# Kernel tuning notes

Hardware: AMD Instinct MI355X
Metric: run time of the kernel (lower is better)

## Reference

```python
import jax, jax.numpy as jnp
import numpy as np
import math

N = 8192  # base points
M = 8192  # target points
FEAT = 5
DESC = 4
HID = 32


def setup_inputs() -> dict:
    key = jax.random.key(0)
    ks = jax.random.split(key, 16)
    s = lambda fan_in: 1.0 / np.sqrt(fan_in)
    return {
        "base_pos": jax.random.normal(ks[0], (N, 2), jnp.float32),
        "base_feat": jax.random.normal(ks[1], (N, FEAT), jnp.float32),
        "base_desc": jax.random.normal(ks[2], (DESC,), jnp.float32),
        "target_pos": jax.random.normal(ks[3], (M, 2), jnp.float32),
        "target_feat": jax.random.normal(ks[4], (M, FEAT), jnp.float32),
        "target_desc": jax.random.normal(ks[5], (DESC,), jnp.float32),
        # NodeWeightNet MLP params (Linear(5,32) -> ReLU -> Linear(32,1))
        "w1": jax.random.uniform(ks[6], (FEAT, HID), jnp.float32, -s(FEAT), s(FEAT)),
        "b1": jax.random.uniform(ks[7], (HID,), jnp.float32, -s(FEAT), s(FEAT)),
        "w2": jax.random.uniform(ks[8], (HID, 1), jnp.float32, -s(HID), s(HID)),
        "b2": jax.random.uniform(ks[9], (1,), jnp.float32, -s(HID), s(HID)),
        # descriptor gate params (Linear(4,32) -> ReLU -> Linear(32,1))
        "g1": jax.random.uniform(ks[10], (DESC, HID), jnp.float32, -s(DESC), s(DESC)),
        "gb1": jax.random.uniform(ks[11], (HID,), jnp.float32, -s(DESC), s(DESC)),
        "g2": jax.random.uniform(ks[12], (HID, 1), jnp.float32, -s(HID), s(HID)),
        "gb2": jax.random.uniform(ks[13], (1,), jnp.float32, -s(HID), s(HID)),
        "log_sigma": jnp.asarray(math.log(0.1), jnp.float32),
        "log_scale": jnp.zeros((2,), jnp.float32),
        "bias": jnp.zeros((1,), jnp.float32),
    }


def _node_weights(feat, w1, b1, w2, b2):
    logits = jax.nn.relu(feat @ w1 + b1) @ w2 + b2  # [N,1]
    w = jax.nn.softplus(logits) + 1e-6
    return (w / w.sum())[:, 0]  # [N], sums to 1


def _mmd_term(x, wx, y, wy, inv_two_sigma2):
    # weighted sum of Gaussian kernel over all pairs, via sq-dist expansion
    d2 = (
        (x * x).sum(-1)[:, None]
        + (y * y).sum(-1)[None, :]
        - 2.0 * (x @ y.T)
    )
    k = jnp.exp(-d2 * inv_two_sigma2)
    return jnp.einsum("i,ij,j->", wx, k, wy)


def reference(base_pos, base_feat, base_desc, target_pos, target_feat, target_desc,
              w1, b1, w2, b2, g1, gb1, g2, gb2, log_sigma, log_scale, bias):
    scale = jnp.exp(log_scale)
    bp = base_pos * scale
    tp = target_pos * scale
    sigma = jnp.exp(log_sigma)
    bw = _node_weights(base_feat, w1, b1, w2, b2)
    tw = _node_weights(target_feat, w1, b1, w2, b2)
    # center=True: subtract each cloud's weighted mean
    bp = bp - (bw[:, None] * bp).sum(0)
    tp = tp - (tw[:, None] * tp).sum(0)
    inv = 1.0 / (2.0 * sigma * sigma)
    loss = (
        _mmd_term(bp, bw, bp, bw, inv)
        - 2.0 * _mmd_term(bp, bw, tp, tw, inv)
        + _mmd_term(tp, tw, tp, tw, inv)
    )
    diff = jnp.abs(base_desc - target_desc)  # [4]
    gate = jax.nn.softplus(jax.nn.relu(diff @ g1 + gb1) @ g2 + gb2) + 1e-6  # [1]
    return loss * gate.squeeze() + bias.squeeze()
```

## Files before the change

kernel.cpp:

```cpp
#include <hip/hip_runtime.h>
#include <math.h>


#define MMD_THREADS 256
#define I_PER_THREAD 4
#define NPTS_PER_BLOCK (MMD_THREADS * I_PER_THREAD)
#define TJ 256

__device__ __forceinline__ float softplusf(float x) {
    return fmaxf(x, 0.0f) + log1pf(expf(-fabsf(x)));
}

__device__ __forceinline__ float fast_exp2(float x) {
#if __has_builtin(__builtin_amdgcn_exp2f)
    return __builtin_amdgcn_exp2f(x);
#else
    return exp2f(x);
#endif
}

__global__ __launch_bounds__(256) void weight_kernel(
    const float* __restrict__ bpos, const float* __restrict__ bfeat,
    const float* __restrict__ tpos, const float* __restrict__ tfeat,
    const float* __restrict__ w1, const float* __restrict__ b1,
    const float* __restrict__ w2, const float* __restrict__ b2,
    const float* __restrict__ log_scale,
    float4* __restrict__ b4, float4* __restrict__ t4,
    float* __restrict__ sums, int n, int m)
{
    int idx = blockIdx.x * 256 + threadIdx.x;
    int total = n + m;
    float w = 0.f, px = 0.f, py = 0.f;
    int cloud = 0;
    if (idx < total) {
        const float* pos; const float* feat; int i;
        if (idx < n) { pos = bpos; feat = bfeat; i = idx; cloud = 0; }
        else         { pos = tpos; feat = tfeat; i = idx - n; cloud = 1; }
        float sx = expf(log_scale[0]);
        float sy = expf(log_scale[1]);
        px = pos[2*i]   * sx;
        py = pos[2*i+1] * sy;
        float f0 = feat[5*i], f1 = feat[5*i+1], f2 = feat[5*i+2],
              f3 = feat[5*i+3], f4 = feat[5*i+4];
        float logit = b2[0];
        #pragma unroll
        for (int h = 0; h < 32; ++h) {
            float a = b1[h];
            a = fmaf(f0, w1[h],      a);
            a = fmaf(f1, w1[32+h],   a);
            a = fmaf(f2, w1[64+h],   a);
            a = fmaf(f3, w1[96+h],   a);
            a = fmaf(f4, w1[128+h],  a);
            a = fmaxf(a, 0.f);
            logit = fmaf(a, w2[h], logit);
        }
        w = softplusf(logit) + 1e-6f;
        float4 v = make_float4(px, py, w, 0.f);
        if (cloud == 0) b4[i] = v; else t4[i] = v;
    }
    float sw = w, swx = w*px, swy = w*py;
    #pragma unroll
    for (int off = 32; off > 0; off >>= 1) {
        sw  += __shfl_down(sw,  off, 64);
        swx += __shfl_down(swx, off, 64);
        swy += __shfl_down(swy, off, 64);
    }
    if ((threadIdx.x & 63) == 0 && idx < total) {
        float* dst = sums + 3 + cloud * 3;
        atomicAdd(dst + 0, sw);
        atomicAdd(dst + 1, swx);
        atomicAdd(dst + 2, swy);
    }
}

__global__ __launch_bounds__(256) void center_kernel(
    float4* __restrict__ b4, float4* __restrict__ t4,
    const float* __restrict__ sums, int n, int m)
{
    int idx = blockIdx.x * 256 + threadIdx.x;
    int total = n + m;
    if (idx >= total) return;
    int cloud = (idx < n) ? 0 : 1;
    float4* arr = cloud ? t4 : b4;
    int i = cloud ? idx - n : idx;
    const float* s = sums + 3 + cloud * 3;
    float sw = s[0];
    float mx = s[1] / sw, my = s[2] / sw;
    float4 v = arr[i];
    arr[i] = make_float4(v.x - mx, v.y - my, v.z / sw, 0.f);
}

__global__ __launch_bounds__(MMD_THREADS) void mmd_kernel(
    const float4* __restrict__ b4, const float4* __restrict__ t4,
    const float* __restrict__ log_sigma,
    float* __restrict__ sums, int n, int m)
{
    int t = blockIdx.z;
    const float4* X; const float4* Y; int nx, ny;
    if (t == 0)      { X = b4; Y = b4; nx = n; ny = n; }
    else if (t == 1) { X = b4; Y = t4; nx = n; ny = m; }
    else             { X = t4; Y = t4; nx = m; ny = m; }
    float sigma = expf(log_sigma[0]);
    float cexp = -1.4426950408889634f / (2.f * sigma * sigma);

    __shared__ float4 ytile[TJ];
    int j0 = blockIdx.y * TJ;
    for (int j = threadIdx.x; j < TJ; j += MMD_THREADS) {
        int jj = j0 + j;
        ytile[j] = (jj < ny) ? Y[jj] : make_float4(0.f, 0.f, 0.f, 0.f);
    }
    __syncthreads();

    float xi[I_PER_THREAD], yi[I_PER_THREAD], wi[I_PER_THREAD], acc[I_PER_THREAD];
    int ibase = blockIdx.x * NPTS_PER_BLOCK + threadIdx.x;
    #pragma unroll
    for (int s = 0; s < I_PER_THREAD; ++s) {
        int ii = ibase + s * MMD_THREADS;
        float4 v = (ii < nx) ? X[ii] : make_float4(0.f, 0.f, 0.f, 0.f);
        xi[s] = v.x; yi[s] = v.y; wi[s] = v.z; acc[s] = 0.f;
    }
    for (int j = 0; j < TJ; ++j) {
        float4 v = ytile[j];
        #pragma unroll
        for (int s = 0; s < I_PER_THREAD; ++s) {
            float dx = xi[s] - v.x;
            float dy = yi[s] - v.y;
            float d2 = fmaf(dy, dy, dx * dx);
            acc[s] = fmaf(v.z, fast_exp2(d2 * cexp), acc[s]);
        }
    }
    float r = 0.f;
    #pragma unroll
    for (int s = 0; s < I_PER_THREAD; ++s) r = fmaf(wi[s], acc[s], r);

    #pragma unroll
    for (int off = 32; off > 0; off >>= 1) r += __shfl_down(r, off, 64);
    __shared__ float wsum[MMD_THREADS / 64];
    int wid = threadIdx.x >> 6;
    if ((threadIdx.x & 63) == 0) wsum[wid] = r;
    __syncthreads();
    if (threadIdx.x == 0) {
        float tot = 0.f;
        #pragma unroll
        for (int k = 0; k < MMD_THREADS / 64; ++k) tot += wsum[k];
        atomicAdd(&sums[t], tot);
    }
}

__global__ void final_kernel(
    const float* __restrict__ bdesc, const float* __restrict__ tdesc,
    const float* __restrict__ g1, const float* __restrict__ gb1,
    const float* __restrict__ g2, const float* __restrict__ gb2,
    const float* __restrict__ bias, const float* __restrict__ sums,
    float* __restrict__ out)
{
    if (threadIdx.x != 0 || blockIdx.x != 0) return;
    float d0 = fabsf(bdesc[0] - tdesc[0]);
    float d1 = fabsf(bdesc[1] - tdesc[1]);
    float d2 = fabsf(bdesc[2] - tdesc[2]);
    float d3 = fabsf(bdesc[3] - tdesc[3]);
    float logit = gb2[0];
    #pragma unroll
    for (int h = 0; h < 32; ++h) {
        float a = gb1[h];
        a = fmaf(d0, g1[h],      a);
        a = fmaf(d1, g1[32+h],   a);
        a = fmaf(d2, g1[64+h],   a);
        a = fmaf(d3, g1[96+h],   a);
        a = fmaxf(a, 0.f);
        logit = fmaf(a, g2[h], logit);
    }
    float gate = softplusf(logit) + 1e-6f;
    float loss = sums[0] - 2.f * sums[1] + sums[2];
    out[0] = loss * gate + bias[0];
}

extern "C" void kernel_launch(void* const* d_in, const int* in_sizes, int n_in,
                              void* d_out, int out_size, void* d_ws, size_t ws_size,
                              hipStream_t stream)
{
    const float* bpos      = (const float*)d_in[0];
    const float* bfeat     = (const float*)d_in[1];
    const float* bdesc     = (const float*)d_in[2];
    const float* tpos      = (const float*)d_in[3];
    const float* tfeat     = (const float*)d_in[4];
    const float* tdesc     = (const float*)d_in[5];
    const float* w1        = (const float*)d_in[6];
    const float* b1        = (const float*)d_in[7];
    const float* w2        = (const float*)d_in[8];
    const float* b2        = (const float*)d_in[9];
    const float* g1        = (const float*)d_in[10];
    const float* gb1       = (const float*)d_in[11];
    const float* g2        = (const float*)d_in[12];
    const float* gb2       = (const float*)d_in[13];
    const float* log_sigma = (const float*)d_in[14];
    const float* log_scale = (const float*)d_in[15];
    const float* bias      = (const float*)d_in[16];
    float* out = (float*)d_out;

    int n = in_sizes[0] / 2;
    int m = in_sizes[3] / 2;

    char* ws = (char*)d_ws;
    float4* b4  = (float4*)ws;
    float4* t4  = (float4*)(ws + (size_t)n * sizeof(float4));
    float* sums = (float*)(ws + (size_t)(n + m) * sizeof(float4));

    hipMemsetAsync(sums, 0, 9 * sizeof(float), stream);

    int total = n + m;
    int wb = (total + 255) / 256;
    weight_kernel<<<wb, 256, 0, stream>>>(bpos, bfeat, tpos, tfeat,
                                          w1, b1, w2, b2, log_scale,
                                          b4, t4, sums, n, m);
    center_kernel<<<wb, 256, 0, stream>>>(b4, t4, sums, n, m);

    int nmax = n > m ? n : m;
    dim3 grid((nmax + NPTS_PER_BLOCK - 1) / NPTS_PER_BLOCK,
              (nmax + TJ - 1) / TJ, 3);
    mmd_kernel<<<grid, MMD_THREADS, 0, stream>>>(b4, t4, log_sigma, sums, n, m);

    final_kernel<<<1, 64, 0, stream>>>(bdesc, tdesc, g1, gb1, g2, gb2,
                                       bias, sums, out);
}
```

Before: 146.6 us.

## Fold sigma into positions, drop center kernel, spread atomics over partial slots

Positions are prescaled by sqrt(log2 e)/sigma so the inner loop computes exp2 of a negated squared distance directly, with no constant multiply. The separate centering pass is removed: the self terms are translation invariant, the cross term applies the difference of the two weighted means, and normalisation by the weight sums moves into the final kernel. The MMD kernel now handles one i-point per thread and reads Y straight from global memory (wave-uniform broadcast) instead of a shared tile, and atomics are spread over 16 partial slots per term. The risk is lower per-thread ILP and fewer points per block, which means more blocks and more reduction overhead.

```diff
diff --git a/kernel.cpp b/kernel.cpp
--- a/kernel.cpp
+++ b/kernel.cpp
@@ -2,10 +2,11 @@
 #include <math.h>
 
 
+#define WK_THREADS 256
 #define MMD_THREADS 256
-#define I_PER_THREAD 4
-#define NPTS_PER_BLOCK (MMD_THREADS * I_PER_THREAD)
-#define TJ 256
+#define IB 256
+#define JB 256
+#define NPART 16
 
 __device__ __forceinline__ float softplusf(float x) {
     return fmaxf(x, 0.0f) + log1pf(expf(-fabsf(x)));
@@ -19,16 +20,16 @@
 #endif
 }
 
-__global__ __launch_bounds__(256) void weight_kernel(
+__global__ __launch_bounds__(WK_THREADS) void weight_kernel(
     const float* __restrict__ bpos, const float* __restrict__ bfeat,
     const float* __restrict__ tpos, const float* __restrict__ tfeat,
     const float* __restrict__ w1, const float* __restrict__ b1,
     const float* __restrict__ w2, const float* __restrict__ b2,
-    const float* __restrict__ log_scale,
+    const float* __restrict__ log_sigma, const float* __restrict__ log_scale,
     float4* __restrict__ b4, float4* __restrict__ t4,
     float* __restrict__ sums, int n, int m)
 {
-    int idx = blockIdx.x * 256 + threadIdx.x;
+    int idx = blockIdx.x * WK_THREADS + threadIdx.x;
     int total = n + m;
     float w = 0.f, px = 0.f, py = 0.f;
     int cloud = 0;
@@ -36,8 +37,10 @@
         const float* pos; const float* feat; int i;
         if (idx < n) { pos = bpos; feat = bfeat; i = idx; cloud = 0; }
         else         { pos = tpos; feat = tfeat; i = idx - n; cloud = 1; }
-        float sx = expf(log_scale[0]);
-        float sy = expf(log_scale[1]);
+        float sigma = expf(log_sigma[0]);
+        float u = 0.8493218003f / sigma;
+        float sx = expf(log_scale[0]) * u;
+        float sy = expf(log_scale[1]) * u;
         px = pos[2*i]   * sx;
         py = pos[2*i+1] * sy;
         float f0 = feat[5*i], f1 = feat[5*i+1], f2 = feat[5*i+2],
@@ -73,65 +76,46 @@
     }
 }
 
-__global__ __launch_bounds__(256) void center_kernel(
-    float4* __restrict__ b4, float4* __restrict__ t4,
-    const float* __restrict__ sums, int n, int m)
-{
-    int idx = blockIdx.x * 256 + threadIdx.x;
-    int total = n + m;
-    if (idx >= total) return;
-    int cloud = (idx < n) ? 0 : 1;
-    float4* arr = cloud ? t4 : b4;
-    int i = cloud ? idx - n : idx;
-    const float* s = sums + 3 + cloud * 3;
-    float sw = s[0];
-    float mx = s[1] / sw, my = s[2] / sw;
-    float4 v = arr[i];
-    arr[i] = make_float4(v.x - mx, v.y - my, v.z / sw, 0.f);
-}
-
 __global__ __launch_bounds__(MMD_THREADS) void mmd_kernel(
     const float4* __restrict__ b4, const float4* __restrict__ t4,
-    const float* __restrict__ log_sigma,
-    float* __restrict__ sums, int n, int m)
+    const float* __restrict__ sums, float* __restrict__ partial,
+    int n, int m)
 {
     int t = blockIdx.z;
     const float4* X; const float4* Y; int nx, ny;
     if (t == 0)      { X = b4; Y = b4; nx = n; ny = n; }
     else if (t == 1) { X = b4; Y = t4; nx = n; ny = m; }
     else             { X = t4; Y = t4; nx = m; ny = m; }
-    float sigma = expf(log_sigma[0]);
-    float cexp = -1.4426950408889634f / (2.f * sigma * sigma);
-
-    __shared__ float4 ytile[TJ];
-    int j0 = blockIdx.y * TJ;
-    for (int j = threadIdx.x; j < TJ; j += MMD_THREADS) {
-        int jj = j0 + j;
-        ytile[j] = (jj < ny) ? Y[jj] : make_float4(0.f, 0.f, 0.f, 0.f);
-    }
-    __syncthreads();
-
-    float xi[I_PER_THREAD], yi[I_PER_THREAD], wi[I_PER_THREAD], acc[I_PER_THREAD];
-    int ibase = blockIdx.x * NPTS_PER_BLOCK + threadIdx.x;
-    #pragma unroll
-    for (int s = 0; s < I_PER_THREAD; ++s) {
-        int ii = ibase + s * MMD_THREADS;
-        float4 v = (ii < nx) ? X[ii] : make_float4(0.f, 0.f, 0.f, 0.f);
-        xi[s] = v.x; yi[s] = v.y; wi[s] = v.z; acc[s] = 0.f;
-    }
-    for (int j = 0; j < TJ; ++j) {
-        float4 v = ytile[j];
-        #pragma unroll
-        for (int s = 0; s < I_PER_THREAD; ++s) {
-            float dx = xi[s] - v.x;
-            float dy = yi[s] - v.y;
-            float d2 = fmaf(dy, dy, dx * dx);
-            acc[s] = fmaf(v.z, fast_exp2(d2 * cexp), acc[s]);
-        }
-    }
-    float r = 0.f;
-    #pragma unroll
-    for (int s = 0; s < I_PER_THREAD; ++s) r = fmaf(wi[s], acc[s], r);
+
+    int ibase = blockIdx.x * IB;
+    int j0 = blockIdx.y * JB;
+    if (ibase >= nx || j0 >= ny) return;
+
+    float dx0 = 0.f, dy0 = 0.f;
+    if (t == 1) {
+        float sb = sums[3], st = sums[6];
+        dx0 = sums[4] / sb - sums[7] / st;
+        dy0 = sums[5] / sb - sums[8] / st;
+    }
+
+    int i = ibase + threadIdx.x;
+    float xi = 0.f, yi = 0.f, wi = 0.f;
+    if (i < nx) {
+        float4 v = X[i];
+        xi = v.x - dx0; yi = v.y - dy0; wi = v.z;
+    }
+
+    int jn = min(JB, ny - j0);
+    const float4* Yp = Y + j0;
+    float acc = 0.f;
+    for (int j = 0; j < jn; ++j) {
+        float4 q = Yp[j];
+        float dx = xi - q.x;
+        float dy = yi - q.y;
+        float e = fast_exp2(fmaf(dy, -dy, -(dx * dx)));
+        acc = fmaf(q.z, e, acc);
+    }
+    float r = wi * acc;
 
     #pragma unroll
     for (int off = 32; off > 0; off >>= 1) r += __shfl_down(r, off, 64);
@@ -143,7 +127,7 @@
         float tot = 0.f;
         #pragma unroll
         for (int k = 0; k < MMD_THREADS / 64; ++k) tot += wsum[k];
-        atomicAdd(&sums[t], tot);
+        atomicAdd(&partial[t * NPART + (blockIdx.x & (NPART - 1))], tot);
     }
 }
 
@@ -152,9 +136,20 @@
     const float* __restrict__ g1, const float* __restrict__ gb1,
     const float* __restrict__ g2, const float* __restrict__ gb2,
     const float* __restrict__ bias, const float* __restrict__ sums,
-    float* __restrict__ out)
+    const float* __restrict__ partial, float* __restrict__ out)
 {
     if (threadIdx.x != 0 || blockIdx.x != 0) return;
+    float P[3];
+    #pragma unroll
+    for (int t = 0; t < 3; ++t) {
+        float s = 0.f;
+        #pragma unroll
+        for (int k = 0; k < NPART; ++k) s += partial[t * NPART + k];
+        P[t] = s;
+    }
+    float sb = sums[3], st = sums[6];
+    float loss = P[0] / (sb * sb) - 2.f * P[1] / (sb * st) + P[2] / (st * st);
+
     float d0 = fabsf(bdesc[0] - tdesc[0]);
     float d1 = fabsf(bdesc[1] - tdesc[1]);
     float d2 = fabsf(bdesc[2] - tdesc[2]);
@@ -171,7 +166,6 @@
         logit = fmaf(a, g2[h], logit);
     }
     float gate = softplusf(logit) + 1e-6f;
-    float loss = sums[0] - 2.f * sums[1] + sums[2];
     out[0] = loss * gate + bias[0];
 }
 
@@ -202,24 +196,23 @@
     int m = in_sizes[3] / 2;
 
     char* ws = (char*)d_ws;
-    float4* b4  = (float4*)ws;
-    float4* t4  = (float4*)(ws + (size_t)n * sizeof(float4));
-    float* sums = (float*)(ws + (size_t)(n + m) * sizeof(float4));
-
-    hipMemsetAsync(sums, 0, 9 * sizeof(float), stream);
+    float4* b4   = (float4*)ws;
+    float4* t4   = (float4*)(ws + (size_t)n * sizeof(float4));
+    float* sums  = (float*)(ws + (size_t)(n + m) * sizeof(float4));
+    float* partial = sums + 9;
+
+    hipMemsetAsync(sums, 0, (9 + 3 * NPART) * sizeof(float), stream);
 
     int total = n + m;
-    int wb = (total + 255) / 256;
-    weight_kernel<<<wb, 256, 0, stream>>>(bpos, bfeat, tpos, tfeat,
-                                          w1, b1, w2, b2, log_scale,
-                                          b4, t4, sums, n, m);
-    center_kernel<<<wb, 256, 0, stream>>>(b4, t4, sums, n, m);
+    int wb = (total + WK_THREADS - 1) / WK_THREADS;
+    weight_kernel<<<wb, WK_THREADS, 0, stream>>>(
+        bpos, bfeat, tpos, tfeat, w1, b1, w2, b2, log_sigma, log_scale,
+        b4, t4, sums, n, m);
 
     int nmax = n > m ? n : m;
-    dim3 grid((nmax + NPTS_PER_BLOCK - 1) / NPTS_PER_BLOCK,
-              (nmax + TJ - 1) / TJ, 3);
-    mmd_kernel<<<grid, MMD_THREADS, 0, stream>>>(b4, t4, log_sigma, sums, n, m);
+    dim3 grid((nmax + IB - 1) / IB, (nmax + JB - 1) / JB, 3);
+    mmd_kernel<<<grid, MMD_THREADS, 0, stream>>>(b4, t4, sums, partial, n, m);
 
     final_kernel<<<1, 64, 0, stream>>>(bdesc, tdesc, g1, gb1, g2, gb2,
-                                       bias, sums, out);
-}
+                                       bias, sums, partial, out);
+}
```

Measured after the change: 157.4 us. +7.4%, slower.
